# Performance work log

Measured on AMD Instinct MI355X. Metric: run time of the kernel, lower is better.

The kernel has to match this reference:

```python
import jax, jax.numpy as jnp
import numpy as np

B, M = 4, 32768            # scenes, candidate slots
A = B * (M // 2)           # static number of active points per group
CINS = (64, 128)           # per-group input channels
HID, COUT = 128, 256       # cfg.mlps = [128, 256]
EPS = 1e-5                 # BatchNorm eps


def setup_inputs() -> dict:
    key = jax.random.key(0)
    ks = jax.random.split(key, 12)
    # hard mask: first M//2 columns of every row active -> exactly A True entries
    mask = jnp.tile(jnp.arange(M) < (M // 2), (B, 1))
    inp = {
        "feats0": jax.random.normal(ks[0], (CINS[0], A), jnp.float32),
        "feats1": jax.random.normal(ks[1], (CINS[1], A), jnp.float32),
        "prob0": jax.random.uniform(ks[2], (B, M), jnp.float32),
        "prob1": jax.random.uniform(ks[3], (B, M), jnp.float32),
        "mask0": mask,
        "mask1": mask,
    }
    for g, cin in enumerate(CINS):
        inp[f"Wa{g}"] = jax.random.normal(ks[4 + 2 * g], (HID, cin), jnp.float32) * 0.05
        inp[f"ga{g}"] = jnp.ones((HID,), jnp.float32)
        inp[f"ba{g}"] = jnp.zeros((HID,), jnp.float32)
        inp[f"Wb{g}"] = jax.random.normal(ks[5 + 2 * g], (COUT, HID), jnp.float32) * 0.05
        inp[f"gb{g}"] = jnp.ones((COUT,), jnp.float32)
        inp[f"bb{g}"] = jnp.zeros((COUT,), jnp.float32)
    return inp


def _bn_relu(x, gamma, beta):
    # training-mode BatchNorm1d over the length axis (N=1), biased variance like torch
    mu = x.mean(axis=1, keepdims=True)
    var = x.var(axis=1, keepdims=True)
    y = (x - mu) * jax.lax.rsqrt(var + EPS) * gamma[:, None] + beta[:, None]
    return jax.nn.relu(y)


def _group(feats, prob, mask, Wa, ga, ba, Wb, gb, bb):
    # 1x1 Conv1d == matmul over channels
    h = _bn_relu(Wa @ feats, ga, ba)          # (HID, A)
    y = _bn_relu(Wb @ h, gb, bb)              # (COUT, A)
    # masked scatter into dense (COUT, B*M) zero tensor, row-major like torch bool indexing
    idx = jnp.nonzero(mask.reshape(-1), size=A)[0]
    full = jnp.zeros((COUT, B * M), y.dtype).at[:, idx].set(y)
    # training-time soft-mask weighting by prob, broadcast over channels
    return full.reshape(COUT, B, M) * prob[None]


def reference(feats0, feats1, prob0, prob1, mask0, mask1,
              Wa0, ga0, ba0, Wb0, gb0, bb0,
              Wa1, ga1, ba1, Wb1, gb1, bb1):
    f0 = _group(feats0, prob0, mask0, Wa0, ga0, ba0, Wb0, gb0, bb0)
    f1 = _group(feats1, prob1, mask1, Wa1, ga1, ba1, Wb1, gb1, bb1)
    # sum over groups, then (C,B,M) -> (B,C,M)
    return (f0 + f1).transpose(1, 0, 2)
```

## Files before the change

kernel.cpp:

```cpp
#include <hip/hip_runtime.h>


#define AT 65536

typedef __bf16 bf16_t;
typedef bf16_t bf16x8 __attribute__((ext_vector_type(8)));
typedef bf16_t bf16x4 __attribute__((ext_vector_type(4)));
typedef float  f32x4  __attribute__((ext_vector_type(4)));

__device__ __forceinline__ f32x4 mfma16(bf16x8 a, bf16x8 b, f32x4 c) {
  return __builtin_amdgcn_mfma_f32_16x16x32_bf16(a, b, c, 0, 0, 0);
}

__device__ __forceinline__ float redcol16(float v) {
  v += __shfl_xor(v, 1, 64);
  v += __shfl_xor(v, 2, 64);
  v += __shfl_xor(v, 4, 64);
  v += __shfl_xor(v, 8, 64);
  return v;
}

__global__ __launch_bounds__(256) void prep_weights(
    const float* __restrict__ Wa0, const float* __restrict__ Wa1,
    const float* __restrict__ Wb0, const float* __restrict__ Wb1,
    bf16_t* __restrict__ Wab0, bf16_t* __restrict__ Wab1,
    bf16_t* __restrict__ Wbb0, bf16_t* __restrict__ Wbb1)
{
  const int i = threadIdx.x + blockIdx.x * 256;
  if (i >= 90112) return;
  if (i < 8192)        Wab0[i]         = (bf16_t)Wa0[i];
  else if (i < 24576)  Wab1[i - 8192]  = (bf16_t)Wa1[i - 8192];
  else if (i < 57344)  Wbb0[i - 24576] = (bf16_t)Wb0[i - 24576];
  else                 Wbb1[i - 57344] = (bf16_t)Wb1[i - 57344];
}

template <int CIN>
__global__ __launch_bounds__(256) void trans_stats(
    const float* __restrict__ feats, const bf16_t* __restrict__ Wab,
    float* __restrict__ Zpart, bf16_t* __restrict__ fT)
{
  constexpr int KS1  = CIN / 32;
  constexpr int GR   = CIN / 8;
  constexpr int ROWB = CIN * 2;
  __shared__ __align__(16) char tile[64 * ROWB];

  const int tid = threadIdx.x, lane = tid & 63;
  const int lr = lane & 15, lk = lane >> 4, wid = tid >> 6;
  const int a0 = (int)blockIdx.x * 64;

  f32x4 v[CIN / 16];
  const int cb = tid >> 4, aq = (tid & 15) * 4;
#pragma unroll
  for (int cc = 0; cc < CIN / 16; ++cc)
    v[cc] = *reinterpret_cast<const f32x4*>(
        feats + (size_t)(cc * 16 + cb) * AT + a0 + aq);

#pragma unroll
  for (int cc = 0; cc < CIN / 16; ++cc) {
    const int c = cc * 16 + cb;
    const int gsw = c >> 3, cbyte = (c & 7) * 2;
#pragma unroll
    for (int i = 0; i < 4; ++i) {
      const int a = aq + i;
      *reinterpret_cast<bf16_t*>(
          tile + a * ROWB + ((gsw ^ (a & 7)) << 4) + cbyte) = (bf16_t)v[cc][i];
    }
  }
  __syncthreads();

  {
    const int g = tid % GR, ar = tid / GR;
#pragma unroll
    for (int i = 0; i < (GR * 64) / 256; ++i) {
      const int a = ar + (256 / GR) * i;
      const bf16x8 w = *reinterpret_cast<const bf16x8*>(
          tile + a * ROWB + ((g ^ (a & 7)) << 4));
      *reinterpret_cast<bf16x8*>(fT + (size_t)(a0 + a) * CIN + g * 8) = w;
    }
  }

  bf16x8 WaF[2][KS1];
#pragma unroll
  for (int mi = 0; mi < 2; ++mi) {
    const bf16_t* base = Wab + (size_t)((2 * wid + mi) * 16 + lr) * CIN + lk * 8;
#pragma unroll
    for (int ks = 0; ks < KS1; ++ks)
      WaF[mi][ks] = *reinterpret_cast<const bf16x8*>(base + ks * 32);
  }

  float zs[2][4] = {}, zq[2][4] = {};
#pragma unroll
  for (int nt = 0; nt < 4; ++nt) {
    const int col = lr + 16 * nt;
    f32x4 z0 = {0.f, 0.f, 0.f, 0.f}, z1 = {0.f, 0.f, 0.f, 0.f};
#pragma unroll
    for (int ks = 0; ks < KS1; ++ks) {
      const int g = ks * 4 + lk;
      const bf16x8 bfr = *reinterpret_cast<const bf16x8*>(
          tile + col * ROWB + ((g ^ (col & 7)) << 4));
      z0 = mfma16(WaF[0][ks], bfr, z0);
      z1 = mfma16(WaF[1][ks], bfr, z1);
    }
#pragma unroll
    for (int i = 0; i < 4; ++i) {
      zs[0][i] += z0[i]; zq[0][i] += z0[i] * z0[i];
      zs[1][i] += z1[i]; zq[1][i] += z1[i] * z1[i];
    }
  }
#pragma unroll
  for (int mi = 0; mi < 2; ++mi) {
#pragma unroll
    for (int i = 0; i < 4; ++i) {
      zs[mi][i] = redcol16(zs[mi][i]);
      zq[mi][i] = redcol16(zq[mi][i]);
    }
    float vs = zs[mi][0], vq = zq[mi][0];
    vs = ((lr & 3) == 1) ? zs[mi][1] : vs;  vq = ((lr & 3) == 1) ? zq[mi][1] : vq;
    vs = ((lr & 3) == 2) ? zs[mi][2] : vs;  vq = ((lr & 3) == 2) ? zq[mi][2] : vq;
    vs = ((lr & 3) == 3) ? zs[mi][3] : vs;  vq = ((lr & 3) == 3) ? zq[mi][3] : vq;
    const float vv = (lr & 4) ? vq : vs;
    if (lr < 8)
      Zpart[(size_t)blockIdx.x * 256 + (lr >> 2) * 128 +
            (2 * wid + mi) * 16 + lk * 4 + (lr & 3)] = vv;
  }
}

__global__ void reduce_fin(const float* __restrict__ part, int nblk, int stride,
                           int nch, const float* __restrict__ gamma,
                           const float* __restrict__ beta,
                           float* __restrict__ scale, float* __restrict__ shift)
{
  const int c = blockIdx.x;
  const int t = threadIdx.x;
  float s = 0.f, q = 0.f;
  for (int b = t; b < nblk; b += 64) {
    s += part[(size_t)b * stride + c];
    q += part[(size_t)b * stride + nch + c];
  }
#pragma unroll
  for (int o = 1; o < 64; o <<= 1) {
    s += __shfl_xor(s, o, 64);
    q += __shfl_xor(q, o, 64);
  }
  if (t == 0) {
    const float inv = 1.f / 65536.f;
    const float mu  = s * inv;
    const float var = q * inv - mu * mu;
    const float sc  = gamma[c] * rsqrtf(var + 1e-5f);
    scale[c] = sc;
    shift[c] = beta[c] - mu * sc;
  }
}

template <int CIN>
__device__ __forceinline__ void gemm1_dev(
    const bf16_t* __restrict__ fT, const bf16_t* __restrict__ Wab,
    const float* __restrict__ scZ, const float* __restrict__ shZ,
    char* __restrict__ hw, int colbase, int lr, int lk)
{
  constexpr int KS = CIN / 32;

  bf16x8 bf[2][KS];
#pragma unroll
  for (int sub = 0; sub < 2; ++sub)
#pragma unroll
    for (int ks = 0; ks < KS; ++ks)
      bf[sub][ks] = *reinterpret_cast<const bf16x8*>(
          fT + (size_t)(colbase + sub * 16 + lr) * CIN + lk * 8 + ks * 32);

#pragma unroll 2
  for (int rb = 0; rb < 8; ++rb) {
    bf16x8 af[KS];
    const bf16_t* wa = Wab + (size_t)(rb * 16 + lr) * CIN + lk * 8;
#pragma unroll
    for (int ks = 0; ks < KS; ++ks)
      af[ks] = *reinterpret_cast<const bf16x8*>(wa + ks * 32);

    f32x4 acc[2];
    acc[0] = f32x4{0.f, 0.f, 0.f, 0.f};
    acc[1] = f32x4{0.f, 0.f, 0.f, 0.f};
#pragma unroll
    for (int ks = 0; ks < KS; ++ks) {
      acc[0] = mfma16(af[ks], bf[0][ks], acc[0]);
      acc[1] = mfma16(af[ks], bf[1][ks], acc[1]);
    }

    const f32x4 sv = *reinterpret_cast<const f32x4*>(scZ + rb * 16 + lk * 4);
    const f32x4 bv = *reinterpret_cast<const f32x4*>(shZ + rb * 16 + lk * 4);
#pragma unroll
    for (int sub = 0; sub < 2; ++sub) {
      bf16x4 hv;
#pragma unroll
      for (int i = 0; i < 4; ++i)
        hv[i] = (bf16_t)fmaxf(acc[sub][i] * sv[i] + bv[i], 0.f);
      const int col = sub * 16 + lr;
      const int g8  = rb * 2 + (lk >> 1);
      *reinterpret_cast<bf16x4*>(
          hw + col * 256 + ((g8 ^ (col & 7)) << 4) + ((lk & 1) << 3)) = hv;
    }
  }
}

template <int PHASE>
__global__ __launch_bounds__(256) void fused_pass(
    const bf16_t* __restrict__ fT0, const bf16_t* __restrict__ fT1,
    const bf16_t* __restrict__ Wab0, const bf16_t* __restrict__ Wab1,
    const bf16_t* __restrict__ Wbb0, const bf16_t* __restrict__ Wbb1,
    const float* __restrict__ prob0, const float* __restrict__ prob1,
    const float* __restrict__ scaleZ, const float* __restrict__ shiftZ,
    const float* __restrict__ scaleY, const float* __restrict__ shiftY,
    float* __restrict__ Ypart, float* __restrict__ out)
{
  __shared__ __align__(16) char hbuf[4][2][8192];
  __shared__ float sstat[(PHASE == 2) ? 1024 : 4];

  const int tid = threadIdx.x, wid = tid >> 6, lane = tid & 63;
  const int lr = lane & 15, lk = lane >> 4;
  const int colbase = (int)blockIdx.x * 128 + wid * 32;

  if constexpr (PHASE == 2) {
    sstat[tid] = 0.f; sstat[tid + 256] = 0.f;
    sstat[tid + 512] = 0.f; sstat[tid + 768] = 0.f;
  }

  gemm1_dev<64>(fT0, Wab0, scaleZ, shiftZ, &hbuf[wid][0][0], colbase, lr, lk);
  gemm1_dev<128>(fT1, Wab1, scaleZ + 128, shiftZ + 128, &hbuf[wid][1][0],
                 colbase, lr, lk);

  if constexpr (PHASE == 2) __syncthreads();

  float p0v[2] = {0.f, 0.f}, p1v[2] = {0.f, 0.f};
  const int bC = (colbase >> 14) * 256;
  const int m0 = colbase & 16383;
  if constexpr (PHASE == 3) {
    const int b = colbase >> 14;
#pragma unroll
    for (int sub = 0; sub < 2; ++sub) {
      const int mm = m0 + sub * 16 + lr;
      p0v[sub] = prob0[((size_t)b << 15) + mm];
      p1v[sub] = prob1[((size_t)b << 15) + mm];
    }
  }

#pragma unroll 2
  for (int rb2 = 0; rb2 < 16; ++rb2) {
    bf16x8 a0f[4], a1f[4];
    const bf16_t* w0 = Wbb0 + (size_t)(rb2 * 16 + lr) * 128 + lk * 8;
    const bf16_t* w1 = Wbb1 + (size_t)(rb2 * 16 + lr) * 128 + lk * 8;
#pragma unroll
    for (int ks = 0; ks < 4; ++ks) {
      a0f[ks] = *reinterpret_cast<const bf16x8*>(w0 + ks * 32);
      a1f[ks] = *reinterpret_cast<const bf16x8*>(w1 + ks * 32);
    }

    f32x4 acc0[2], acc1[2];
    acc0[0] = f32x4{0.f, 0.f, 0.f, 0.f}; acc0[1] = f32x4{0.f, 0.f, 0.f, 0.f};
    acc1[0] = f32x4{0.f, 0.f, 0.f, 0.f}; acc1[1] = f32x4{0.f, 0.f, 0.f, 0.f};
#pragma unroll
    for (int ks2 = 0; ks2 < 4; ++ks2) {
#pragma unroll
      for (int sub = 0; sub < 2; ++sub) {
        const int col = sub * 16 + lr;
        const int off = col * 256 + (((ks2 * 4 + lk) ^ (col & 7)) << 4);
        const bf16x8 h0 = *reinterpret_cast<const bf16x8*>(&hbuf[wid][0][0] + off);
        acc0[sub] = mfma16(a0f[ks2], h0, acc0[sub]);
        const bf16x8 h1 = *reinterpret_cast<const bf16x8*>(&hbuf[wid][1][0] + off);
        acc1[sub] = mfma16(a1f[ks2], h1, acc1[sub]);
      }
    }

    if constexpr (PHASE == 2) {
#pragma unroll
      for (int g = 0; g < 2; ++g) {
        const f32x4* ac = g ? acc1 : acc0;
        float s[4], q[4];
#pragma unroll
        for (int i = 0; i < 4; ++i) {
          s[i] = redcol16(ac[0][i] + ac[1][i]);
          q[i] = redcol16(ac[0][i] * ac[0][i] + ac[1][i] * ac[1][i]);
        }
        float vs = s[0], vq = q[0];
        vs = ((lr & 3) == 1) ? s[1] : vs;  vq = ((lr & 3) == 1) ? q[1] : vq;
        vs = ((lr & 3) == 2) ? s[2] : vs;  vq = ((lr & 3) == 2) ? q[2] : vq;
        vs = ((lr & 3) == 3) ? s[3] : vs;  vq = ((lr & 3) == 3) ? q[3] : vq;
        const float vv = (lr & 4) ? vq : vs;
        if (lr < 8)
          atomicAdd(&sstat[g * 512 + ((lr >> 2) << 8) +
                           rb2 * 16 + lk * 4 + (lr & 3)], vv);
      }
    } else {
      const f32x4 sv0 = *reinterpret_cast<const f32x4*>(scaleY + rb2 * 16 + lk * 4);
      const f32x4 bv0 = *reinterpret_cast<const f32x4*>(shiftY + rb2 * 16 + lk * 4);
      const f32x4 sv1 = *reinterpret_cast<const f32x4*>(scaleY + 256 + rb2 * 16 + lk * 4);
      const f32x4 bv1 = *reinterpret_cast<const f32x4*>(shiftY + 256 + rb2 * 16 + lk * 4);
#pragma unroll
      for (int sub = 0; sub < 2; ++sub) {
        const int mm = m0 + sub * 16 + lr;
#pragma unroll
        for (int i = 0; i < 4; ++i) {
          const int ch = rb2 * 16 + lk * 4 + i;
          const float v =
              fmaxf(acc0[sub][i] * sv0[i] + bv0[i], 0.f) * p0v[sub] +
              fmaxf(acc1[sub][i] * sv1[i] + bv1[i], 0.f) * p1v[sub];
          float* op = out + (((size_t)(bC + ch)) << 15) + mm;
          op[0] = v;
          op[16384] = 0.f;
        }
      }
    }
  }

  if constexpr (PHASE == 2) {
    __syncthreads();
#pragma unroll
    for (int j = 0; j < 4; ++j)
      Ypart[(size_t)blockIdx.x * 1024 + j * 256 + tid] = sstat[j * 256 + tid];
  }
}

extern "C" void kernel_launch(void* const* d_in, const int* in_sizes, int n_in,
                              void* d_out, int out_size, void* d_ws, size_t ws_size,
                              hipStream_t stream)
{
  (void)in_sizes; (void)n_in; (void)out_size; (void)ws_size;
  const float* feats0 = (const float*)d_in[0];
  const float* feats1 = (const float*)d_in[1];
  const float* prob0  = (const float*)d_in[2];
  const float* prob1  = (const float*)d_in[3];
  const float* Wa0 = (const float*)d_in[6];
  const float* ga0 = (const float*)d_in[7];
  const float* ba0 = (const float*)d_in[8];
  const float* Wb0 = (const float*)d_in[9];
  const float* gb0 = (const float*)d_in[10];
  const float* bb0 = (const float*)d_in[11];
  const float* Wa1 = (const float*)d_in[12];
  const float* ga1 = (const float*)d_in[13];
  const float* ba1 = (const float*)d_in[14];
  const float* Wb1 = (const float*)d_in[15];
  const float* gb1 = (const float*)d_in[16];
  const float* bb1 = (const float*)d_in[17];

  float* out = (float*)d_out;
  char*  wsb = (char*)d_ws;

  float* scaleZ = (float*)wsb;
  float* shiftZ = scaleZ + 256;
  float* scaleY = shiftZ + 256;
  float* shiftY = scaleY + 512;
  bf16_t* Wab0 = (bf16_t*)(wsb + (8   << 10));
  bf16_t* Wab1 = (bf16_t*)(wsb + (24  << 10));
  bf16_t* Wbb0 = (bf16_t*)(wsb + (56  << 10));
  bf16_t* Wbb1 = (bf16_t*)(wsb + (120 << 10));
  float* ZpartG0 = (float*)(wsb + (192 << 10));
  float* ZpartG1 = (float*)(wsb + (192 << 10) + (1 << 20));
  float* Ypart   = ZpartG0;
  bf16_t* fT0 = (bf16_t*)(wsb + (2304 << 10));
  bf16_t* fT1 = (bf16_t*)(wsb + (2304 << 10) + (8 << 20));

  prep_weights<<<352, 256, 0, stream>>>(Wa0, Wa1, Wb0, Wb1,
                                        Wab0, Wab1, Wbb0, Wbb1);

  trans_stats<64><<<1024, 256, 0, stream>>>(feats0, Wab0, ZpartG0, fT0);
  trans_stats<128><<<1024, 256, 0, stream>>>(feats1, Wab1, ZpartG1, fT1);

  reduce_fin<<<128, 64, 0, stream>>>(ZpartG0, 1024, 256, 128, ga0, ba0,
                                     scaleZ, shiftZ);
  reduce_fin<<<128, 64, 0, stream>>>(ZpartG1, 1024, 256, 128, ga1, ba1,
                                     scaleZ + 128, shiftZ + 128);

  fused_pass<2><<<512, 256, 0, stream>>>(fT0, fT1, Wab0, Wab1, Wbb0, Wbb1,
      prob0, prob1, scaleZ, shiftZ, scaleY, shiftY, Ypart, out);

  reduce_fin<<<256, 64, 0, stream>>>(Ypart, 512, 1024, 256, gb0, bb0,
                                     scaleY, shiftY);
  reduce_fin<<<256, 64, 0, stream>>>(Ypart + 512, 512, 1024, 256, gb1, bb1,
                                     scaleY + 256, shiftY + 256);

  fused_pass<3><<<512, 256, 0, stream>>>(fT0, fT1, Wab0, Wab1, Wbb0, Wbb1,
      prob0, prob1, scaleZ, shiftZ, scaleY, shiftY, Ypart, out);
}
```

Before: 168.6 us.

## Materialize pre-BN output once and replace partial-sum reductions with atomics

The second GEMM now runs once. Its pre-normalization output is stored as bf16, and a separate elementwise pass applies BN, ReLU, prob weighting and zero fill with vectorized coalesced stores. Per-block stat partials and reduce kernels are replaced by global atomic accumulation, and the per-group launches are merged. This avoids recomputing both GEMMs in the output phase and cuts launch count, at the cost of extra intermediate memory traffic, atomic contention and a bf16 rounding of Y before normalization.

After: 350.6 us. 108% more time.

```diff
diff --git a/kernel.cpp b/kernel.cpp
--- a/kernel.cpp
+++ b/kernel.cpp
@@ -24,29 +24,29 @@
     const float* __restrict__ Wa0, const float* __restrict__ Wa1,
     const float* __restrict__ Wb0, const float* __restrict__ Wb1,
     bf16_t* __restrict__ Wab0, bf16_t* __restrict__ Wab1,
-    bf16_t* __restrict__ Wbb0, bf16_t* __restrict__ Wbb1)
+    bf16_t* __restrict__ Wbb0, bf16_t* __restrict__ Wbb1,
+    float* __restrict__ stats)
 {
   const int i = threadIdx.x + blockIdx.x * 256;
-  if (i >= 90112) return;
   if (i < 8192)        Wab0[i]         = (bf16_t)Wa0[i];
   else if (i < 24576)  Wab1[i - 8192]  = (bf16_t)Wa1[i - 8192];
   else if (i < 57344)  Wbb0[i - 24576] = (bf16_t)Wb0[i - 24576];
-  else                 Wbb1[i - 57344] = (bf16_t)Wb1[i - 57344];
+  else if (i < 90112)  Wbb1[i - 57344] = (bf16_t)Wb1[i - 57344];
+  else if (i < 91648)  stats[i - 90112] = 0.f;
 }
 
 template <int CIN>
-__global__ __launch_bounds__(256) void trans_stats(
+__device__ __forceinline__ void trans_one(
     const float* __restrict__ feats, const bf16_t* __restrict__ Wab,
-    float* __restrict__ Zpart, bf16_t* __restrict__ fT)
+    float* __restrict__ zsum, float* __restrict__ zssq,
+    bf16_t* __restrict__ fT, int blk, char* __restrict__ tile)
 {
   constexpr int KS1  = CIN / 32;
   constexpr int GR   = CIN / 8;
   constexpr int ROWB = CIN * 2;
-  __shared__ __align__(16) char tile[64 * ROWB];
-
   const int tid = threadIdx.x, lane = tid & 63;
   const int lr = lane & 15, lk = lane >> 4, wid = tid >> 6;
-  const int a0 = (int)blockIdx.x * 64;
+  const int a0 = blk * 64;
 
   f32x4 v[CIN / 16];
   const int cb = tid >> 4, aq = (tid & 15) * 4;
@@ -95,9 +95,9 @@
     f32x4 z0 = {0.f, 0.f, 0.f, 0.f}, z1 = {0.f, 0.f, 0.f, 0.f};
 #pragma unroll
     for (int ks = 0; ks < KS1; ++ks) {
-      const int g = ks * 4 + lk;
+      const int g2 = ks * 4 + lk;
       const bf16x8 bfr = *reinterpret_cast<const bf16x8*>(
-          tile + col * ROWB + ((g ^ (col & 7)) << 4));
+          tile + col * ROWB + ((g2 ^ (col & 7)) << 4));
       z0 = mfma16(WaF[0][ks], bfr, z0);
       z1 = mfma16(WaF[1][ks], bfr, z1);
     }
@@ -119,37 +119,47 @@
     vs = ((lr & 3) == 2) ? zs[mi][2] : vs;  vq = ((lr & 3) == 2) ? zq[mi][2] : vq;
     vs = ((lr & 3) == 3) ? zs[mi][3] : vs;  vq = ((lr & 3) == 3) ? zq[mi][3] : vq;
     const float vv = (lr & 4) ? vq : vs;
-    if (lr < 8)
-      Zpart[(size_t)blockIdx.x * 256 + (lr >> 2) * 128 +
-            (2 * wid + mi) * 16 + lk * 4 + (lr & 3)] = vv;
-  }
-}
-
-__global__ void reduce_fin(const float* __restrict__ part, int nblk, int stride,
-                           int nch, const float* __restrict__ gamma,
-                           const float* __restrict__ beta,
-                           float* __restrict__ scale, float* __restrict__ shift)
-{
-  const int c = blockIdx.x;
+    if (lr < 8) {
+      const int ch = (2 * wid + mi) * 16 + lk * 4 + (lr & 3);
+      atomicAdd(((lr & 4) ? zssq : zsum) + ch, vv);
+    }
+  }
+}
+
+__global__ __launch_bounds__(256) void trans_stats_all(
+    const float* __restrict__ feats0, const float* __restrict__ feats1,
+    const bf16_t* __restrict__ Wab0, const bf16_t* __restrict__ Wab1,
+    float* __restrict__ zsum, float* __restrict__ zssq,
+    bf16_t* __restrict__ fT0, bf16_t* __restrict__ fT1)
+{
+  __shared__ __align__(16) char tile[64 * 256];
+  if (blockIdx.x < 1024)
+    trans_one<64>(feats0, Wab0, zsum, zssq, fT0, blockIdx.x, tile);
+  else
+    trans_one<128>(feats1, Wab1, zsum + 128, zssq + 128, fT1,
+                   blockIdx.x - 1024, tile);
+}
+
+__global__ void finalize_stats(const float* __restrict__ sum,
+                               const float* __restrict__ ssq,
+                               const float* __restrict__ gamma0,
+                               const float* __restrict__ beta0,
+                               const float* __restrict__ gamma1,
+                               const float* __restrict__ beta1,
+                               float* __restrict__ scale,
+                               float* __restrict__ shift, int nch)
+{
   const int t = threadIdx.x;
-  float s = 0.f, q = 0.f;
-  for (int b = t; b < nblk; b += 64) {
-    s += part[(size_t)b * stride + c];
-    q += part[(size_t)b * stride + nch + c];
-  }
-#pragma unroll
-  for (int o = 1; o < 64; o <<= 1) {
-    s += __shfl_xor(s, o, 64);
-    q += __shfl_xor(q, o, 64);
-  }
-  if (t == 0) {
-    const float inv = 1.f / 65536.f;
-    const float mu  = s * inv;
-    const float var = q * inv - mu * mu;
-    const float sc  = gamma[c] * rsqrtf(var + 1e-5f);
-    scale[c] = sc;
-    shift[c] = beta[c] - mu * sc;
-  }
+  const int g = t / nch;
+  const int c = t - g * nch;
+  const float inv = 1.f / 65536.f;
+  const float mu  = sum[t] * inv;
+  const float var = ssq[t] * inv - mu * mu;
+  const float ga  = (g ? gamma1 : gamma0)[c];
+  const float be  = (g ? beta1 : beta0)[c];
+  const float sc  = ga * rsqrtf(var + 1e-5f);
+  scale[t] = sc;
+  shift[t] = be - mu * sc;
 }
 
 template <int CIN>
@@ -201,120 +211,119 @@
   }
 }
 
-template <int PHASE>
-__global__ __launch_bounds__(256) void fused_pass(
+__device__ __forceinline__ void gemm2_store(
+    const char* __restrict__ hw, const bf16_t* __restrict__ Wbb,
+    float* __restrict__ ysum, float* __restrict__ yssq,
+    bf16_t* __restrict__ Y, int colbase, int lr, int lk)
+{
+#pragma unroll 2
+  for (int rb2 = 0; rb2 < 16; ++rb2) {
+    bf16x8 af[4];
+    const bf16_t* w = Wbb + (size_t)(rb2 * 16 + lr) * 128 + lk * 8;
+#pragma unroll
+    for (int ks = 0; ks < 4; ++ks)
+      af[ks] = *reinterpret_cast<const bf16x8*>(w + ks * 32);
+
+    f32x4 acc[2];
+    acc[0] = f32x4{0.f, 0.f, 0.f, 0.f};
+    acc[1] = f32x4{0.f, 0.f, 0.f, 0.f};
+#pragma unroll
+    for (int ks2 = 0; ks2 < 4; ++ks2) {
+#pragma unroll
+      for (int sub = 0; sub < 2; ++sub) {
+        const int col = sub * 16 + lr;
+        const int off = col * 256 + (((ks2 * 4 + lk) ^ (col & 7)) << 4);
+        const bf16x8 hf = *reinterpret_cast<const bf16x8*>(hw + off);
+        acc[sub] = mfma16(af[ks2], hf, acc[sub]);
+      }
+    }
+
+#pragma unroll
+    for (int sub = 0; sub < 2; ++sub) {
+      const int a = colbase + sub * 16 + lr;
+#pragma unroll
+      for (int i = 0; i < 4; ++i)
+        Y[(size_t)(rb2 * 16 + lk * 4 + i) * AT + a] = (bf16_t)acc[sub][i];
+    }
+
+    float s[4], q[4];
+#pragma unroll
+    for (int i = 0; i < 4; ++i) {
+      s[i] = redcol16(acc[0][i] + acc[1][i]);
+      q[i] = redcol16(acc[0][i] * acc[0][i] + acc[1][i] * acc[1][i]);
+    }
+    float vs = s[0], vq = q[0];
+    vs = ((lr & 3) == 1) ? s[1] : vs;  vq = ((lr & 3) == 1) ? q[1] : vq;
+    vs = ((lr & 3) == 2) ? s[2] : vs;  vq = ((lr & 3) == 2) ? q[2] : vq;
+    vs = ((lr & 3) == 3) ? s[3] : vs;  vq = ((lr & 3) == 3) ? q[3] : vq;
+    const float vv = (lr & 4) ? vq : vs;
+    if (lr < 8) {
+      const int ch = rb2 * 16 + lk * 4 + (lr & 3);
+      atomicAdd(((lr & 4) ? yssq : ysum) + ch, vv);
+    }
+  }
+}
+
+__global__ __launch_bounds__(256) void mid_pass(
     const bf16_t* __restrict__ fT0, const bf16_t* __restrict__ fT1,
     const bf16_t* __restrict__ Wab0, const bf16_t* __restrict__ Wab1,
     const bf16_t* __restrict__ Wbb0, const bf16_t* __restrict__ Wbb1,
-    const float* __restrict__ prob0, const float* __restrict__ prob1,
     const float* __restrict__ scaleZ, const float* __restrict__ shiftZ,
-    const float* __restrict__ scaleY, const float* __restrict__ shiftY,
-    float* __restrict__ Ypart, float* __restrict__ out)
-{
-  __shared__ __align__(16) char hbuf[4][2][8192];
-  __shared__ float sstat[(PHASE == 2) ? 1024 : 4];
-
+    float* __restrict__ ysum, float* __restrict__ yssq,
+    bf16_t* __restrict__ Y0, bf16_t* __restrict__ Y1)
+{
+  __shared__ __align__(16) char hbuf[4][8192];
   const int tid = threadIdx.x, wid = tid >> 6, lane = tid & 63;
   const int lr = lane & 15, lk = lane >> 4;
   const int colbase = (int)blockIdx.x * 128 + wid * 32;
-
-  if constexpr (PHASE == 2) {
-    sstat[tid] = 0.f; sstat[tid + 256] = 0.f;
-    sstat[tid + 512] = 0.f; sstat[tid + 768] = 0.f;
-  }
-
-  gemm1_dev<64>(fT0, Wab0, scaleZ, shiftZ, &hbuf[wid][0][0], colbase, lr, lk);
-  gemm1_dev<128>(fT1, Wab1, scaleZ + 128, shiftZ + 128, &hbuf[wid][1][0],
-                 colbase, lr, lk);
-
-  if constexpr (PHASE == 2) __syncthreads();
-
-  float p0v[2] = {0.f, 0.f}, p1v[2] = {0.f, 0.f};
-  const int bC = (colbase >> 14) * 256;
-  const int m0 = colbase & 16383;
-  if constexpr (PHASE == 3) {
-    const int b = colbase >> 14;
-#pragma unroll
-    for (int sub = 0; sub < 2; ++sub) {
-      const int mm = m0 + sub * 16 + lr;
-      p0v[sub] = prob0[((size_t)b << 15) + mm];
-      p1v[sub] = prob1[((size_t)b << 15) + mm];
-    }
-  }
-
-#pragma unroll 2
-  for (int rb2 = 0; rb2 < 16; ++rb2) {
-    bf16x8 a0f[4], a1f[4];
-    const bf16_t* w0 = Wbb0 + (size_t)(rb2 * 16 + lr) * 128 + lk * 8;
-    const bf16_t* w1 = Wbb1 + (size_t)(rb2 * 16 + lr) * 128 + lk * 8;
-#pragma unroll
-    for (int ks = 0; ks < 4; ++ks) {
-      a0f[ks] = *reinterpret_cast<const bf16x8*>(w0 + ks * 32);
-      a1f[ks] = *reinterpret_cast<const bf16x8*>(w1 + ks * 32);
-    }
-
-    f32x4 acc0[2], acc1[2];
-    acc0[0] = f32x4{0.f, 0.f, 0.f, 0.f}; acc0[1] = f32x4{0.f, 0.f, 0.f, 0.f};
-    acc1[0] = f32x4{0.f, 0.f, 0.f, 0.f}; acc1[1] = f32x4{0.f, 0.f, 0.f, 0.f};
-#pragma unroll
-    for (int ks2 = 0; ks2 < 4; ++ks2) {
-#pragma unroll
-      for (int sub = 0; sub < 2; ++sub) {
-        const int col = sub * 16 + lr;
-        const int off = col * 256 + (((ks2 * 4 + lk) ^ (col & 7)) << 4);
-        const bf16x8 h0 = *reinterpret_cast<const bf16x8*>(&hbuf[wid][0][0] + off);
-        acc0[sub] = mfma16(a0f[ks2], h0, acc0[sub]);
-        const bf16x8 h1 = *reinterpret_cast<const bf16x8*>(&hbuf[wid][1][0] + off);
-        acc1[sub] = mfma16(a1f[ks2], h1, acc1[sub]);
-      }
-    }
-
-    if constexpr (PHASE == 2) {
-#pragma unroll
-      for (int g = 0; g < 2; ++g) {
-        const f32x4* ac = g ? acc1 : acc0;
-        float s[4], q[4];
-#pragma unroll
-        for (int i = 0; i < 4; ++i) {
-          s[i] = redcol16(ac[0][i] + ac[1][i]);
-          q[i] = redcol16(ac[0][i] * ac[0][i] + ac[1][i] * ac[1][i]);
-        }
-        float vs = s[0], vq = q[0];
-        vs = ((lr & 3) == 1) ? s[1] : vs;  vq = ((lr & 3) == 1) ? q[1] : vq;
-        vs = ((lr & 3) == 2) ? s[2] : vs;  vq = ((lr & 3) == 2) ? q[2] : vq;
-        vs = ((lr & 3) == 3) ? s[3] : vs;  vq = ((lr & 3) == 3) ? q[3] : vq;
-        const float vv = (lr & 4) ? vq : vs;
-        if (lr < 8)
-          atomicAdd(&sstat[g * 512 + ((lr >> 2) << 8) +
-                           rb2 * 16 + lk * 4 + (lr & 3)], vv);
-      }
-    } else {
-      const f32x4 sv0 = *reinterpret_cast<const f32x4*>(scaleY + rb2 * 16 + lk * 4);
-      const f32x4 bv0 = *reinterpret_cast<const f32x4*>(shiftY + rb2 * 16 + lk * 4);
-      const f32x4 sv1 = *reinterpret_cast<const f32x4*>(scaleY + 256 + rb2 * 16 + lk * 4);
-      const f32x4 bv1 = *reinterpret_cast<const f32x4*>(shiftY + 256 + rb2 * 16 + lk * 4);
-#pragma unroll
-      for (int sub = 0; sub < 2; ++sub) {
-        const int mm = m0 + sub * 16 + lr;
-#pragma unroll
-        for (int i = 0; i < 4; ++i) {
-          const int ch = rb2 * 16 + lk * 4 + i;
-          const float v =
-              fmaxf(acc0[sub][i] * sv0[i] + bv0[i], 0.f) * p0v[sub] +
-              fmaxf(acc1[sub][i] * sv1[i] + bv1[i], 0.f) * p1v[sub];
-          float* op = out + (((size_t)(bC + ch)) << 15) + mm;
-          op[0] = v;
-          op[16384] = 0.f;
-        }
-      }
-    }
-  }
-
-  if constexpr (PHASE == 2) {
-    __syncthreads();
-#pragma unroll
-    for (int j = 0; j < 4; ++j)
-      Ypart[(size_t)blockIdx.x * 1024 + j * 256 + tid] = sstat[j * 256 + tid];
+  char* hw = hbuf[wid];
+
+  gemm1_dev<64>(fT0, Wab0, scaleZ, shiftZ, hw, colbase, lr, lk);
+  gemm2_store(hw, Wbb0, ysum, yssq, Y0, colbase, lr, lk);
+  gemm1_dev<128>(fT1, Wab1, scaleZ + 128, shiftZ + 128, hw, colbase, lr, lk);
+  gemm2_store(hw, Wbb1, ysum + 256, yssq + 256, Y1, colbase, lr, lk);
+}
+
+__global__ __launch_bounds__(256) void final_pass(
+    const bf16_t* __restrict__ Y0, const bf16_t* __restrict__ Y1,
+    const float* __restrict__ prob0, const float* __restrict__ prob1,
+    const float* __restrict__ scaleY, const float* __restrict__ shiftY,
+    float* __restrict__ out)
+{
+  const int gid  = (int)blockIdx.x * 256 + threadIdx.x;
+  const int row  = gid >> 10;
+  const int mseg = (gid & 1023) << 4;
+  const int b = row >> 8, ch = row & 255;
+  const size_t a = ((size_t)b << 14) + mseg;
+
+  const float s0 = scaleY[ch],       h0 = shiftY[ch];
+  const float s1 = scaleY[256 + ch], h1 = shiftY[256 + ch];
+
+  const bf16x8* y0p = reinterpret_cast<const bf16x8*>(Y0 + (size_t)ch * AT + a);
+  const bf16x8* y1p = reinterpret_cast<const bf16x8*>(Y1 + (size_t)ch * AT + a);
+  const bf16x8 y0v[2] = {y0p[0], y0p[1]};
+  const bf16x8 y1v[2] = {y1p[0], y1p[1]};
+
+  const f32x4* p0p = reinterpret_cast<const f32x4*>(prob0 + ((size_t)b << 15) + mseg);
+  const f32x4* p1p = reinterpret_cast<const f32x4*>(prob1 + ((size_t)b << 15) + mseg);
+  f32x4 p0v[4], p1v[4];
+#pragma unroll
+  for (int j = 0; j < 4; ++j) { p0v[j] = p0p[j]; p1v[j] = p1p[j]; }
+
+  f32x4 o[4];
+#pragma unroll
+  for (int j = 0; j < 16; ++j) {
+    const float v0 = fmaxf((float)y0v[j >> 3][j & 7] * s0 + h0, 0.f) * p0v[j >> 2][j & 3];
+    const float v1 = fmaxf((float)y1v[j >> 3][j & 7] * s1 + h1, 0.f) * p1v[j >> 2][j & 3];
+    o[j >> 2][j & 3] = v0 + v1;
+  }
+
+  float* ob = out + ((size_t)row << 15) + mseg;
+  const f32x4 z = {0.f, 0.f, 0.f, 0.f};
+#pragma unroll
+  for (int j = 0; j < 4; ++j) {
+    reinterpret_cast<f32x4*>(ob)[j] = o[j];
+    reinterpret_cast<f32x4*>(ob + 16384)[j] = z;
   }
 }
 
@@ -342,40 +351,40 @@
 
   float* out = (float*)d_out;
   char*  wsb = (char*)d_ws;
-
-  float* scaleZ = (float*)wsb;
-  float* shiftZ = scaleZ + 256;
-  float* scaleY = shiftZ + 256;
-  float* shiftY = scaleY + 512;
-  bf16_t* Wab0 = (bf16_t*)(wsb + (8   << 10));
-  bf16_t* Wab1 = (bf16_t*)(wsb + (24  << 10));
-  bf16_t* Wbb0 = (bf16_t*)(wsb + (56  << 10));
-  bf16_t* Wbb1 = (bf16_t*)(wsb + (120 << 10));
-  float* ZpartG0 = (float*)(wsb + (192 << 10));
-  float* ZpartG1 = (float*)(wsb + (192 << 10) + (1 << 20));
-  float* Ypart   = ZpartG0;
-  bf16_t* fT0 = (bf16_t*)(wsb + (2304 << 10));
-  bf16_t* fT1 = (bf16_t*)(wsb + (2304 << 10) + (8 << 20));
-
-  prep_weights<<<352, 256, 0, stream>>>(Wa0, Wa1, Wb0, Wb1,
-                                        Wab0, Wab1, Wbb0, Wbb1);
-
-  trans_stats<64><<<1024, 256, 0, stream>>>(feats0, Wab0, ZpartG0, fT0);
-  trans_stats<128><<<1024, 256, 0, stream>>>(feats1, Wab1, ZpartG1, fT1);
-
-  reduce_fin<<<128, 64, 0, stream>>>(ZpartG0, 1024, 256, 128, ga0, ba0,
-                                     scaleZ, shiftZ);
-  reduce_fin<<<128, 64, 0, stream>>>(ZpartG1, 1024, 256, 128, ga1, ba1,
-                                     scaleZ + 128, shiftZ + 128);
-
-  fused_pass<2><<<512, 256, 0, stream>>>(fT0, fT1, Wab0, Wab1, Wbb0, Wbb1,
-      prob0, prob1, scaleZ, shiftZ, scaleY, shiftY, Ypart, out);
-
-  reduce_fin<<<256, 64, 0, stream>>>(Ypart, 512, 1024, 256, gb0, bb0,
-                                     scaleY, shiftY);
-  reduce_fin<<<256, 64, 0, stream>>>(Ypart + 512, 512, 1024, 256, gb1, bb1,
-                                     scaleY + 256, shiftY + 256);
-
-  fused_pass<3><<<512, 256, 0, stream>>>(fT0, fT1, Wab0, Wab1, Wbb0, Wbb1,
-      prob0, prob1, scaleZ, shiftZ, scaleY, shiftY, Ypart, out);
-}
+  float* ws  = (float*)d_ws;
+
+  float* zsum = ws;
+  float* zssq = ws + 256;
+  float* ysum = ws + 512;
+  float* yssq = ws + 1024;
+  float* scaleZ = ws + 1536;
+  float* shiftZ = ws + 1792;
+  float* scaleY = ws + 2048;
+  float* shiftY = ws + 2560;
+  bf16_t* Wab0 = (bf16_t*)(wsb + (16  << 10));
+  bf16_t* Wab1 = (bf16_t*)(wsb + (32  << 10));
+  bf16_t* Wbb0 = (bf16_t*)(wsb + (64  << 10));
+  bf16_t* Wbb1 = (bf16_t*)(wsb + (128 << 10));
+  bf16_t* fT0 = (bf16_t*)(wsb + (256 << 10));
+  bf16_t* fT1 = (bf16_t*)(wsb + (256 << 10) + (8 << 20));
+  bf16_t* Y0  = (bf16_t*)(wsb + (32ull << 20));
+  bf16_t* Y1  = (bf16_t*)(wsb + (64ull << 20));
+
+  prep_weights<<<358, 256, 0, stream>>>(Wa0, Wa1, Wb0, Wb1,
+                                        Wab0, Wab1, Wbb0, Wbb1, zsum);
+
+  trans_stats_all<<<2048, 256, 0, stream>>>(feats0, feats1, Wab0, Wab1,
+                                            zsum, zssq, fT0, fT1);
+
+  finalize_stats<<<1, 256, 0, stream>>>(zsum, zssq, ga0, ba0, ga1, ba1,
+                                        scaleZ, shiftZ, 128);
+
+  mid_pass<<<512, 256, 0, stream>>>(fT0, fT1, Wab0, Wab1, Wbb0, Wbb1,
+                                    scaleZ, shiftZ, ysum, yssq, Y0, Y1);
+
+  finalize_stats<<<1, 512, 0, stream>>>(ysum, yssq, gb0, bb0, gb1, bb1,
+                                        scaleY, shiftY, 256);
+
+  final_pass<<<4096, 256, 0, stream>>>(Y0, Y1, prob0, prob1,
+                                       scaleY, shiftY, out);
+}
```
